# Performance work log

Hardware: AMD Instinct MI355X
Metric: run time of the kernel (lower is better)

## Reference

```python
import jax, jax.numpy as jnp
from jax import lax
import numpy as np

SMOOTH = 1e-05
BASE_W = jnp.array([1.0, 1.0, 1.0], dtype=jnp.float32)
BOUND_W = jnp.array([2.0, 3.0, 5.0], dtype=jnp.float32)
FG_W = jnp.array([1.0, 1.5, 3.0], dtype=jnp.float32)
MAX_DIST = 10.0  # cv2 result is clamped to 10.0 in the original module
R = 10  # search radius: any distance > 10 is clamped anyway

# Precompute all integer offsets with Euclidean norm <= R (includes (0,0) -> dist 0)
_offs = [(dy, dx, float(np.hypot(dy, dx)))
         for dy in range(-R, R + 1) for dx in range(-R, R + 1)
         if dy * dy + dx * dx <= R * R]
_DY = jnp.array([o[0] + R for o in _offs], dtype=jnp.int32)  # shifted into padded coords
_DX = jnp.array([o[1] + R for o in _offs], dtype=jnp.int32)
_DD = jnp.array([o[2] for o in _offs], dtype=jnp.float32)


def _distance_transform(mask):
    """Clamped Euclidean distance from each pixel to the nearest foreground pixel.
    mask: [B,H,W] binary float (1 = foreground). Equivalent to
    clamp(cv2.distanceTransform(1-mask, DIST_L2), max=10) (exact L2 vs chamfer approx).
    """
    B, H, W = mask.shape
    pad = jnp.pad(mask, ((0, 0), (R, R), (R, R)))

    def step(cur, od):
        dy, dx, d = od
        sl = lax.dynamic_slice(pad, (0, dy, dx), (B, H, W))
        return jnp.minimum(cur, jnp.where(sl > 0.5, d, MAX_DIST)), None

    init = jnp.full((B, H, W), MAX_DIST, dtype=mask.dtype)
    dist, _ = lax.scan(step, init, (_DY, _DX, _DD))
    return dist


def setup_inputs() -> dict:
    key = jax.random.key(0)
    k1, k2, k3 = jax.random.split(key, 3)
    B, H, W = 64, 512, 512
    predictions = jax.random.normal(k1, (B, 1, H, W), dtype=jnp.float32)
    targets = (jax.random.uniform(k2, (B, 1, H, W)) < 0.2).astype(jnp.float32)
    task_ids = jax.random.randint(k3, (B,), 0, 3)
    return {"predictions": predictions, "targets": targets, "task_ids": task_ids}


def reference(predictions, targets, task_ids):
    x, t = predictions, targets
    axes = (1, 2, 3)
    p = jax.nn.sigmoid(x)
    pc = jnp.clip(p, 1e-07, 1.0 - 1e-07)

    # ---- base loss: per-sample Dice + BCEWithLogits ----
    inter = jnp.sum(pc * t, axis=axes)
    union = jnp.sum(pc, axis=axes) + jnp.sum(t, axis=axes)
    dice_loss = 1.0 - (2.0 * inter + SMOOTH) / (union + SMOOTH)
    # numerically stable BCE-with-logits
    bce = jnp.maximum(x, 0.0) - x * t + jnp.log1p(jnp.exp(-jnp.abs(x)))
    base_loss = dice_loss + jnp.mean(bce, axis=axes)

    # ---- boundary loss: distance-transform weighted L1 ----
    tb = (t > 0.5).astype(x.dtype)  # [B,1,H,W]
    dist = _distance_transform(tb[:, 0])  # [B,H,W], clamped at 10
    boundary_loss = jnp.mean(dist * jnp.abs(pc[:, 0] - tb[:, 0]), axis=(1, 2))

    # ---- foreground-weighted BCE ----
    fg = tb
    bg = 1.0 - tb
    fg_count = jnp.sum(fg, axis=axes)
    bg_count = jnp.sum(bg, axis=axes)
    fg_weight = jnp.clip(bg_count / (fg_count + 1e-07), 1.0, 10.0)
    bce_p = -(t * jnp.log(pc) + (1.0 - t) * jnp.log(1.0 - pc))
    w = fg * fg_weight[:, None, None, None] + bg
    fg_loss = jnp.mean(bce_p * w, axis=axes)
    fg_loss = jnp.where(fg_count == 0, 0.0, fg_loss)

    per_sample = (BASE_W[task_ids] * base_loss
                  + BOUND_W[task_ids] * boundary_loss
                  + FG_W[task_ids] * fg_loss)
    return jnp.mean(per_sample)
```

## Files before the change

### kernel.cpp

```cpp
#include <hip/hip_runtime.h>
#include <stdint.h>

#define NB 64
#define NH 512
#define NW 512
#define RPAD 10
#define NROWS (NH + 2 * RPAD)
#define RWORDS 18
#define IMG_WORDS (NROWS * RWORDS)
#define NPIX (NH * NW)

#if __has_builtin(__builtin_amdgcn_alignbit)
#define ALIGNBIT(hi, lo, s) __builtin_amdgcn_alignbit((hi), (lo), (s))
#else
#define ALIGNBIT(hi, lo, s) ((uint32_t)(((((uint64_t)(hi)) << 32) | (lo)) >> ((s) & 31)))
#endif

template <int N>
__device__ __forceinline__ float dpp_add(float v) {
#if __has_builtin(__builtin_amdgcn_update_dpp)
    int s = __builtin_amdgcn_update_dpp(0, __float_as_int(v), 0x110 | N, 0xf, 0xf, true);
    return v + __int_as_float(s);
#else
    return v + __shfl_up(v, N, 16);
#endif
}


__global__ __launch_bounds__(256) void build_bits(const float* __restrict__ targ,
                                                  uint32_t* __restrict__ bits,
                                                  float* __restrict__ partials) {
    const int b   = blockIdx.y;
    const int tid = threadIdx.x;
    const int wave = tid >> 6, lane = tid & 63;
    const int r = blockIdx.x * 4 + wave;
    const int y = r - RPAD;

    if (blockIdx.x == 0 && b == 0) {
        partials[tid] = 0.0f;
        partials[tid + 256] = 0.0f;
    }

    uint32_t m = 0;
    if (y >= 0 && y < NH) {
        const float4* tg = (const float4*)(targ + ((size_t)b * NH + y) * NW + lane * 8);
        const float4 a = tg[0];
        const float4 c = tg[1];
        m = (uint32_t)(a.x > 0.5f)
          | ((uint32_t)(a.y > 0.5f) << 1)
          | ((uint32_t)(a.z > 0.5f) << 2)
          | ((uint32_t)(a.w > 0.5f) << 3)
          | ((uint32_t)(c.x > 0.5f) << 4)
          | ((uint32_t)(c.y > 0.5f) << 5)
          | ((uint32_t)(c.z > 0.5f) << 6)
          | ((uint32_t)(c.w > 0.5f) << 7);
    }

    __shared__ uint32_t swd[4][16];
    ((uint8_t*)swd[wave])[lane] = (uint8_t)m;
    __syncthreads();
    if (lane < RWORDS) {
        const uint32_t v = (lane >= 1 && lane <= 16) ? swd[wave][lane - 1] : 0u;
        bits[(size_t)b * IMG_WORDS + (size_t)r * RWORDS + lane] = v;
    }
}

__global__ __launch_bounds__(256) void main_loss(const float* __restrict__ pred,
                                                 const uint32_t* __restrict__ bits,
                                                 float* __restrict__ partials) {
    const int y0 = blockIdx.x * 4;
    const int b  = blockIdx.y;
    const int tid  = threadIdx.x;
    const int wave = tid >> 6, lane = tid & 63;
    const int y = y0 + wave;
    const int x = lane * 8;

    const float4* pp = (const float4*)(pred + ((size_t)b * NH + y) * NW + x);
    const float4 p0 = pp[0], p1 = pp[1];

    __shared__ uint32_t sb[24 * RWORDS];
    const uint32_t* img = bits + (size_t)b * IMG_WORDS;
    if (tid < 108)
        ((uint4*)sb)[tid] = ((const uint4*)(img + (size_t)y0 * RWORDS))[tid];
    __syncthreads();

    const int lw = (x + 22) >> 5;
    const int s0i = (x + 22) & 31;
    const uint32_t* wrow = sb + wave * RWORDS + lw;

    uint32_t mind2[8];
#pragma unroll
    for (int i = 0; i < 8; ++i) mind2[i] = 1u << 20;

#define FOLD(K2, W32, RV) { \
        _Pragma("unroll") \
        for (int i = 0; i < 8; ++i) { \
            const uint32_t cc = ((W32) >> (10 + i)) | ((RV) >> (21 - i)) | 2048u; \
            const uint32_t dx = (uint32_t)__builtin_ctz(cc); \
            const uint32_t d2 = (uint32_t)(K2) + dx * dx; \
            mind2[i] = min(mind2[i], d2); \
        } }

#define PAIR(K) { \
        const uint32_t lo = wrow[(10 + (K)) * RWORDS]     | wrow[(10 - (K)) * RWORDS]; \
        const uint32_t hi = wrow[(10 + (K)) * RWORDS + 1] | wrow[(10 - (K)) * RWORDS + 1]; \
        const uint32_t w32 = ALIGNBIT(hi, lo, s0i); \
        const uint32_t rv  = __builtin_bitreverse32(w32); \
        FOLD((K) * (K), w32, rv) }

#define CHECK(K) { \
        const uint32_t mx = max(max(max(mind2[0], mind2[1]), max(mind2[2], mind2[3])), \
                                max(max(mind2[4], mind2[5]), max(mind2[6], mind2[7]))); \
        if (__all(mx <= (uint32_t)((K) * (K)))) goto dt_done; }

    uint32_t c32;
    {
        const uint32_t lo = wrow[10 * RWORDS];
        const uint32_t hi = wrow[10 * RWORDS + 1];
        c32 = ALIGNBIT(hi, lo, s0i);
        const uint32_t rv = __builtin_bitreverse32(c32);
        FOLD(0, c32, rv)
    }
    PAIR(1)
    PAIR(2)  CHECK(3)
    PAIR(3)  CHECK(4)
    PAIR(4)  CHECK(5)
    PAIR(5)  CHECK(6)
    PAIR(6)  CHECK(7)
    PAIR(7)  CHECK(8)
    PAIR(8)  CHECK(9)
    PAIR(9)  CHECK(10)
    PAIR(10)
dt_done:;

    const float pv[8] = {p0.x, p0.y, p0.z, p0.w, p1.x, p1.y, p1.z, p1.w};
    float s0 = 0.0f, s1 = 0.0f, s3 = 0.0f, s4 = 0.0f, st = 0.0f;
#pragma unroll
    for (int i = 0; i < 8; ++i) {
        const uint32_t tbb = (c32 >> (10 + i)) & 1u;
        const float tbf = (float)tbb;
        const float xv = pv[i];
        const float e  = __expf(-fabsf(xv));
        const float ope = 1.0f + e;
        const float L  = __logf(ope);
        const float r  = __builtin_amdgcn_rcpf(ope);
        const float p  = (xv >= 0.0f) ? r : 1.0f - r;
        const float dist = __fsqrt_rn((float)min(mind2[i], 100u));
        const float bce = fmaxf(tbb ? -xv : xv, 0.0f) + L;
        s0 = fmaf(tbf, p, s0);
        s1 += p;
        s3 = fmaf(dist, fabsf(p - tbf), s3);
        s4 = fmaf(tbf, bce, s4);
        st += bce;
    }
    const float s2 = (float)__popc(c32 & 0x0003FC00u);
    const float s5 = st - s4;

    float v[6] = {s0, s1, s2, s3, s4, s5};
#pragma unroll
    for (int k = 0; k < 6; ++k) {
        v[k] = dpp_add<1>(v[k]);
        v[k] = dpp_add<2>(v[k]);
        v[k] = dpp_add<4>(v[k]);
        v[k] = dpp_add<8>(v[k]);
    }
    __shared__ float red[16][6];
    if ((lane & 15) == 15) {
        const int g = wave * 4 + (lane >> 4);
#pragma unroll
        for (int k = 0; k < 6; ++k) red[g][k] = v[k];
    }
    __syncthreads();
    if (tid < 6) {
        float acc = 0.0f;
#pragma unroll
        for (int g = 0; g < 16; ++g) acc += red[g][tid];
        atomicAdd(&partials[b * 8 + tid], acc);
    }
}

__global__ __launch_bounds__(64) void finalize(const float* __restrict__ partials,
                                               const int* __restrict__ task_ids,
                                               float* __restrict__ out) {
    const int b = threadIdx.x;
    const float Nf = (float)NPIX;
    const float inter = partials[b * 8 + 0];
    const float spc   = partials[b * 8 + 1];
    const float sfg   = partials[b * 8 + 2];
    const float sbdry = partials[b * 8 + 3];
    const float sfgb  = partials[b * 8 + 4];
    const float sbgb  = partials[b * 8 + 5];

    const float sbce = sfgb + sbgb;
    const float dice = 1.0f - (2.0f * inter + 1e-5f) / (spc + sfg + 1e-5f);
    const float base = dice + sbce / Nf;
    const float bdry = sbdry / Nf;
    const float fgw  = fminf(fmaxf((Nf - sfg) / (sfg + 1e-7f), 1.0f), 10.0f);
    float fgl = (fgw * sfgb + sbgb) / Nf;
    if (sfg == 0.0f) fgl = 0.0f;

    const int t = task_ids[b];
    const float BDW[3] = {2.0f, 3.0f, 5.0f};
    const float FW[3]  = {1.0f, 1.5f, 3.0f};
    float per = base + BDW[t] * bdry + FW[t] * fgl;

#pragma unroll
    for (int off = 32; off > 0; off >>= 1)
        per += __shfl_down(per, off, 64);
    if (b == 0) out[0] = per * (1.0f / 64.0f);
}

extern "C" void kernel_launch(void* const* d_in, const int* in_sizes, int n_in,
                              void* d_out, int out_size, void* d_ws, size_t ws_size,
                              hipStream_t stream) {
    const float* pred     = (const float*)d_in[0];
    const float* targ     = (const float*)d_in[1];
    const int*   task_ids = (const int*)d_in[2];
    float* out = (float*)d_out;

    float* partials = (float*)d_ws;
    uint32_t* bits = (uint32_t*)((char*)d_ws + 4096);

    build_bits<<<dim3(NROWS / 4, NB), 256, 0, stream>>>(targ, bits, partials);
    main_loss<<<dim3(NH / 4, NB), 256, 0, stream>>>(pred, bits, partials);
    finalize<<<1, 64, 0, stream>>>(partials, task_ids, out);
}
```

Before: 156.8 us.

## Fuse target bitmask construction into loss kernel with in-block halo rows

Removes the separate build_bits kernel and its global bitmask buffer. Each block now handles 8 output rows with 512 threads, reads the 28 halo rows of targets directly, and packs them into shared-memory bitmasks. Zeroing the partials moves to hipMemsetAsync. This saves a launch and the round trip of the bitmask through global memory. In exchange, each target row is read by several blocks, about 3.5x redundant target traffic unless caches absorb it.

```diff
diff --git a/kernel.cpp b/kernel.cpp
--- a/kernel.cpp
+++ b/kernel.cpp
@@ -5,9 +5,8 @@
 #define NH 512
 #define NW 512
 #define RPAD 10
-#define NROWS (NH + 2 * RPAD)
 #define RWORDS 18
-#define IMG_WORDS (NROWS * RWORDS)
+#define HROWS 28
 #define NPIX (NH * NW)
 
 #if __has_builtin(__builtin_amdgcn_alignbit)
@@ -27,48 +26,10 @@
 }
 
 
-__global__ __launch_bounds__(256) void build_bits(const float* __restrict__ targ,
-                                                  uint32_t* __restrict__ bits,
+__global__ __launch_bounds__(512) void fused_loss(const float* __restrict__ pred,
+                                                  const float* __restrict__ targ,
                                                   float* __restrict__ partials) {
-    const int b   = blockIdx.y;
-    const int tid = threadIdx.x;
-    const int wave = tid >> 6, lane = tid & 63;
-    const int r = blockIdx.x * 4 + wave;
-    const int y = r - RPAD;
-
-    if (blockIdx.x == 0 && b == 0) {
-        partials[tid] = 0.0f;
-        partials[tid + 256] = 0.0f;
-    }
-
-    uint32_t m = 0;
-    if (y >= 0 && y < NH) {
-        const float4* tg = (const float4*)(targ + ((size_t)b * NH + y) * NW + lane * 8);
-        const float4 a = tg[0];
-        const float4 c = tg[1];
-        m = (uint32_t)(a.x > 0.5f)
-          | ((uint32_t)(a.y > 0.5f) << 1)
-          | ((uint32_t)(a.z > 0.5f) << 2)
-          | ((uint32_t)(a.w > 0.5f) << 3)
-          | ((uint32_t)(c.x > 0.5f) << 4)
-          | ((uint32_t)(c.y > 0.5f) << 5)
-          | ((uint32_t)(c.z > 0.5f) << 6)
-          | ((uint32_t)(c.w > 0.5f) << 7);
-    }
-
-    __shared__ uint32_t swd[4][16];
-    ((uint8_t*)swd[wave])[lane] = (uint8_t)m;
-    __syncthreads();
-    if (lane < RWORDS) {
-        const uint32_t v = (lane >= 1 && lane <= 16) ? swd[wave][lane - 1] : 0u;
-        bits[(size_t)b * IMG_WORDS + (size_t)r * RWORDS + lane] = v;
-    }
-}
-
-__global__ __launch_bounds__(256) void main_loss(const float* __restrict__ pred,
-                                                 const uint32_t* __restrict__ bits,
-                                                 float* __restrict__ partials) {
-    const int y0 = blockIdx.x * 4;
+    const int y0 = blockIdx.x * 8;
     const int b  = blockIdx.y;
     const int tid  = threadIdx.x;
     const int wave = tid >> 6, lane = tid & 63;
@@ -78,10 +39,35 @@
     const float4* pp = (const float4*)(pred + ((size_t)b * NH + y) * NW + x);
     const float4 p0 = pp[0], p1 = pp[1];
 
-    __shared__ uint32_t sb[24 * RWORDS];
-    const uint32_t* img = bits + (size_t)b * IMG_WORDS;
-    if (tid < 108)
-        ((uint4*)sb)[tid] = ((const uint4*)(img + (size_t)y0 * RWORDS))[tid];
+    __shared__ uint32_t sb[HROWS * RWORDS];
+    if (tid < HROWS * 2) {
+        const int hr = tid >> 1;
+        sb[hr * RWORDS + ((tid & 1) ? (RWORDS - 1) : 0)] = 0u;
+    }
+    const float* tgi = targ + (size_t)b * NPIX;
+#pragma unroll
+    for (int k = 0; k < 4; ++k) {
+        const int c = tid + k * 512;
+        if (c < HROWS * 64) {
+            const int hr = c >> 6, xc = c & 63;
+            const int yy = y0 + hr - RPAD;
+            uint32_t m = 0;
+            if (yy >= 0 && yy < NH) {
+                const float4* tg = (const float4*)(tgi + (size_t)yy * NW + xc * 8);
+                const float4 a = tg[0];
+                const float4 d = tg[1];
+                m = (uint32_t)(a.x > 0.5f)
+                  | ((uint32_t)(a.y > 0.5f) << 1)
+                  | ((uint32_t)(a.z > 0.5f) << 2)
+                  | ((uint32_t)(a.w > 0.5f) << 3)
+                  | ((uint32_t)(d.x > 0.5f) << 4)
+                  | ((uint32_t)(d.y > 0.5f) << 5)
+                  | ((uint32_t)(d.z > 0.5f) << 6)
+                  | ((uint32_t)(d.w > 0.5f) << 7);
+            }
+            ((uint8_t*)sb)[hr * (RWORDS * 4) + 4 + xc] = (uint8_t)m;
+        }
+    }
     __syncthreads();
 
     const int lw = (x + 22) >> 5;
@@ -164,7 +150,7 @@
         v[k] = dpp_add<4>(v[k]);
         v[k] = dpp_add<8>(v[k]);
     }
-    __shared__ float red[16][6];
+    __shared__ float red[32][6];
     if ((lane & 15) == 15) {
         const int g = wave * 4 + (lane >> 4);
 #pragma unroll
@@ -174,7 +160,7 @@
     if (tid < 6) {
         float acc = 0.0f;
 #pragma unroll
-        for (int g = 0; g < 16; ++g) acc += red[g][tid];
+        for (int g = 0; g < 32; ++g) acc += red[g][tid];
         atomicAdd(&partials[b * 8 + tid], acc);
     }
 }
@@ -219,9 +205,8 @@
     float* out = (float*)d_out;
 
     float* partials = (float*)d_ws;
-    uint32_t* bits = (uint32_t*)((char*)d_ws + 4096);
-
-    build_bits<<<dim3(NROWS / 4, NB), 256, 0, stream>>>(targ, bits, partials);
-    main_loss<<<dim3(NH / 4, NB), 256, 0, stream>>>(pred, bits, partials);
+
+    hipMemsetAsync(partials, 0, NB * 8 * sizeof(float), stream);
+    fused_loss<<<dim3(NH / 8, NB), 512, 0, stream>>>(pred, targ, partials);
     finalize<<<1, 64, 0, stream>>>(partials, task_ids, out);
 }
```

Result: no change. 157.8 us (+0.7%).
